# Performance work log

Hardware: AMD Instinct MI355X
Metric: run time of the kernel (lower is better)

Reference implementation:

```python
import jax, jax.numpy as jnp
import numpy as np

N_NODES = 100000
N_EDGES = 1200000
D = 64
N_LAYERS = 3
N_GRAPHS = 128


def setup_inputs() -> dict:
    key = jax.random.key(0)
    ks = jax.random.split(key, 8)
    x = jax.random.normal(ks[0], (N_NODES, D), dtype=jnp.float32)
    edge_index = jax.random.randint(ks[1], (2, N_EDGES), 0, N_NODES, dtype=jnp.int32)
    edge_attr = jax.random.normal(ks[2], (N_EDGES, D), dtype=jnp.float32)
    batch = jnp.sort(jax.random.randint(ks[3], (N_NODES,), 0, N_GRAPHS, dtype=jnp.int32))
    scale = 1.0 / np.sqrt(D)
    W1 = jax.random.normal(ks[4], (N_LAYERS, D, D), dtype=jnp.float32) * scale
    b1 = jnp.zeros((N_LAYERS, D), dtype=jnp.float32)
    W2 = jax.random.normal(ks[5], (N_LAYERS, D, D), dtype=jnp.float32) * scale
    b2 = jnp.zeros((N_LAYERS, D), dtype=jnp.float32)
    Wout = jax.random.normal(ks[6], (D, 1), dtype=jnp.float32) * scale
    bout = jnp.zeros((1,), dtype=jnp.float32)
    return {"x": x, "edge_index": edge_index, "edge_attr": edge_attr, "batch": batch,
            "W1": W1, "b1": b1, "W2": W2, "b2": b2, "Wout": Wout, "bout": bout}


def reference(x, edge_index, edge_attr, batch, W1, b1, W2, b2, Wout, bout):
    n_nodes = x.shape[0]
    src, dst = edge_index[0], edge_index[1]  # j -> i (PyG convention)
    for l in range(N_LAYERS):
        # GINEConv: message = ReLU(x_j + e_ij), sum-aggregate, eps=0
        msg = jax.nn.relu(x[src] + edge_attr)              # [E, D]
        aggr = jax.ops.segment_sum(msg, dst, num_segments=n_nodes)  # [N, D]
        h = x + aggr                                        # (1+eps)*x + aggr, eps=0
        # post-aggregation MLP: Linear -> ReLU -> Linear
        h = jax.nn.relu(h @ W1[l] + b1[l]) @ W2[l] + b2[l]
        x = jax.nn.relu(h)                                  # outer ReLU in GINENet.forward
    pooled = jax.ops.segment_sum(x, batch, num_segments=N_GRAPHS)  # global_add_pool
    out = pooled @ Wout + bout                              # [G, 1]
    return out.squeeze(-1)
```

## Files before the change

### kernel.cpp

```cpp
#include <hip/hip_runtime.h>
#include <hip/hip_bf16.h>

#define D 64

typedef unsigned short u16;
typedef unsigned long long u64;
typedef __attribute__((ext_vector_type(8))) unsigned short u16x8;
typedef __attribute__((ext_vector_type(8))) short bf16x8;
typedef __attribute__((ext_vector_type(4))) float f32x4;

static __device__ __forceinline__ u16 f2bf(float f) {
    unsigned u = __float_as_uint(f);
    unsigned r = (u + 0x7FFFu + ((u >> 16) & 1u)) >> 16;
    return (u16)r;
}
static __device__ __forceinline__ float bf2f(u16 h) {
    return __uint_as_float(((unsigned)h) << 16);
}

__global__ void out_init_kernel(float* __restrict__ out, const float* __restrict__ bout, int G) {
    int i = blockIdx.x * blockDim.x + threadIdx.x;
    if (i < G) out[i] = bout[0];
}

__global__ void deg_hist_kernel(const int* __restrict__ ei, int* __restrict__ deg, int E) {
    int e = blockIdx.x * blockDim.x + threadIdx.x;
    if (e < E) atomicAdd(&deg[ei[E + e]], 1);
}

__global__ __launch_bounds__(1024) void scan1_kernel(
    const int* __restrict__ deg, int* __restrict__ off, int* __restrict__ bsum, int N)
{
    __shared__ int sh[1024];
    int t = threadIdx.x;
    int i = blockIdx.x * 1024 + t;
    int v = (i < N) ? deg[i] : 0;
    sh[t] = v;
    __syncthreads();
#pragma unroll
    for (int o = 1; o < 1024; o <<= 1) {
        int u = (t >= o) ? sh[t - o] : 0;
        __syncthreads();
        sh[t] += u;
        __syncthreads();
    }
    if (i < N) off[i] = sh[t] - v;
    if (t == 1023) bsum[blockIdx.x] = sh[t];
}

__global__ __launch_bounds__(128) void scan2_kernel(
    const int* __restrict__ bsum, int* __restrict__ boff, int nb)
{
    __shared__ int sh[128];
    int t = threadIdx.x;
    int v = (t < nb) ? bsum[t] : 0;
    sh[t] = v;
    __syncthreads();
#pragma unroll
    for (int o = 1; o < 128; o <<= 1) {
        int u = (t >= o) ? sh[t - o] : 0;
        __syncthreads();
        sh[t] += u;
        __syncthreads();
    }
    if (t < nb) boff[t] = sh[t] - v;
}

__global__ void scan3_kernel(int* __restrict__ off, const int* __restrict__ boff, int N) {
    int i = blockIdx.x * blockDim.x + threadIdx.x;
    if (i < N) off[i] += boff[i >> 10];
}

__global__ __launch_bounds__(256) void build_kernel(
    const float* __restrict__ ea, const int* __restrict__ ei,
    const int* __restrict__ off, int* __restrict__ cur,
    int* __restrict__ src_csr, u16* __restrict__ ea_csr, int E)
{
    const int lane = threadIdx.x & 63;
    const int q = lane & 15, g = lane >> 4;
    const long long wv = (long long)blockIdx.x * 4 + (threadIdx.x >> 6);
    const int e = (int)(wv * 4) + g;

    int p = 0, s = 0;
    if (e < E && q == 0) {
        int d = ei[E + e];
        s = ei[e];
        p = off[d] + atomicAdd(&cur[d], 1);
    }
    p = __shfl(p, lane & 48, 64);
    if (e >= E) return;

    float4 v = *(const float4*)&ea[(size_t)e * D + q * 4];
    u64 pk = (u64)f2bf(v.x) | ((u64)f2bf(v.y) << 16)
           | ((u64)f2bf(v.z) << 32) | ((u64)f2bf(v.w) << 48);
    __builtin_nontemporal_store(pk, (u64*)&ea_csr[(size_t)p * D + q * 4]);
    if (q == 0) src_csr[p] = s;
}

__global__ __launch_bounds__(256) void convx_kernel(
    const float* __restrict__ xf, u16* __restrict__ xb, long long n4)
{
    long long i = (long long)blockIdx.x * blockDim.x + threadIdx.x;
    if (i >= n4) return;
    float4 v = ((const float4*)xf)[i];
    ushort4 o;
    o.x = f2bf(v.x); o.y = f2bf(v.y); o.z = f2bf(v.z); o.w = f2bf(v.w);
    ((ushort4*)xb)[i] = o;
}

__global__ __launch_bounds__(256) void aggregate_kernel(
    const u16* __restrict__ xbf, const u16* __restrict__ ea_csr,
    const int* __restrict__ src_csr, const int* __restrict__ off,
    const int* __restrict__ deg, u16* __restrict__ hbf, int N)
{
    const int lane = threadIdx.x & 63;
    const int sub  = lane & 7;
    const int g    = lane >> 3;
    const int n = (blockIdx.x << 2) + (threadIdx.x >> 6);
    if (n >= N) return;

    const int p0 = off[n];
    const int dg = deg[n];

    u16x8 xs;
    if (g == 0) xs = *(const u16x8*)&xbf[(size_t)n * D + sub * 8];

    float a0=0.f,a1=0.f,a2=0.f,a3=0.f,a4=0.f,a5=0.f,a6=0.f,a7=0.f;

    if (dg > 0) {
        const int srcAll = src_csr[p0 + min(lane, dg - 1)];
        const int nct = (dg + 7) >> 3;

        int e0 = min(g, dg - 1);
        int sv = __shfl(srcAll, e0, 64);
        int s0 = sv;
        u16x8 evA = *(const u16x8*)&ea_csr[(size_t)(p0 + e0) * D + sub * 8];
        u16x8 xvA = *(const u16x8*)&xbf[(size_t)s0 * D + sub * 8];
        float mA = (g < dg) ? 1.f : 0.f;

        for (int c = 1; c < nct; ++c) {
            int e1 = min(c * 8 + g, dg - 1);
            int sv1 = __shfl(srcAll, e1 & 63, 64);
            int s1 = (e1 < 64) ? sv1 : src_csr[p0 + e1];
            u16x8 evB = *(const u16x8*)&ea_csr[(size_t)(p0 + e1) * D + sub * 8];
            u16x8 xvB = *(const u16x8*)&xbf[(size_t)s1 * D + sub * 8];
            float mB = (c * 8 + g < dg) ? 1.f : 0.f;

            a0 = fmaf(mA, fmaxf(bf2f(xvA[0]) + bf2f(evA[0]), 0.f), a0);
            a1 = fmaf(mA, fmaxf(bf2f(xvA[1]) + bf2f(evA[1]), 0.f), a1);
            a2 = fmaf(mA, fmaxf(bf2f(xvA[2]) + bf2f(evA[2]), 0.f), a2);
            a3 = fmaf(mA, fmaxf(bf2f(xvA[3]) + bf2f(evA[3]), 0.f), a3);
            a4 = fmaf(mA, fmaxf(bf2f(xvA[4]) + bf2f(evA[4]), 0.f), a4);
            a5 = fmaf(mA, fmaxf(bf2f(xvA[5]) + bf2f(evA[5]), 0.f), a5);
            a6 = fmaf(mA, fmaxf(bf2f(xvA[6]) + bf2f(evA[6]), 0.f), a6);
            a7 = fmaf(mA, fmaxf(bf2f(xvA[7]) + bf2f(evA[7]), 0.f), a7);

            xvA = xvB; evA = evB; mA = mB;
        }
        a0 = fmaf(mA, fmaxf(bf2f(xvA[0]) + bf2f(evA[0]), 0.f), a0);
        a1 = fmaf(mA, fmaxf(bf2f(xvA[1]) + bf2f(evA[1]), 0.f), a1);
        a2 = fmaf(mA, fmaxf(bf2f(xvA[2]) + bf2f(evA[2]), 0.f), a2);
        a3 = fmaf(mA, fmaxf(bf2f(xvA[3]) + bf2f(evA[3]), 0.f), a3);
        a4 = fmaf(mA, fmaxf(bf2f(xvA[4]) + bf2f(evA[4]), 0.f), a4);
        a5 = fmaf(mA, fmaxf(bf2f(xvA[5]) + bf2f(evA[5]), 0.f), a5);
        a6 = fmaf(mA, fmaxf(bf2f(xvA[6]) + bf2f(evA[6]), 0.f), a6);
        a7 = fmaf(mA, fmaxf(bf2f(xvA[7]) + bf2f(evA[7]), 0.f), a7);
    }

#pragma unroll
    for (int o = 8; o < 64; o <<= 1) {
        a0 += __shfl_xor(a0, o, 64);  a1 += __shfl_xor(a1, o, 64);
        a2 += __shfl_xor(a2, o, 64);  a3 += __shfl_xor(a3, o, 64);
        a4 += __shfl_xor(a4, o, 64);  a5 += __shfl_xor(a5, o, 64);
        a6 += __shfl_xor(a6, o, 64);  a7 += __shfl_xor(a7, o, 64);
    }

    if (g == 0) {
        u16x8 ho;
        ho[0] = f2bf(a0 + bf2f(xs[0]));
        ho[1] = f2bf(a1 + bf2f(xs[1]));
        ho[2] = f2bf(a2 + bf2f(xs[2]));
        ho[3] = f2bf(a3 + bf2f(xs[3]));
        ho[4] = f2bf(a4 + bf2f(xs[4]));
        ho[5] = f2bf(a5 + bf2f(xs[5]));
        ho[6] = f2bf(a6 + bf2f(xs[6]));
        ho[7] = f2bf(a7 + bf2f(xs[7]));
        *(u16x8*)&hbf[(size_t)n * D + sub * 8] = ho;
    }
}

template <int LAST>
__global__ __launch_bounds__(256) void mlp_mfma_kernel(
    const u16* __restrict__ hbf, u16* __restrict__ xout,
    const float* __restrict__ W1, const float* __restrict__ b1,
    const float* __restrict__ W2, const float* __restrict__ b2,
    const int* __restrict__ batch, const float* __restrict__ Wout,
    float* __restrict__ out, int N, int ntiles)
{
    __shared__ __align__(16) u16 lds_h[4][16][72];
    __shared__ float pool[128];

    const int lane = threadIdx.x & 63;
    const int wid  = threadIdx.x >> 6;
    const int lr   = lane & 15;
    const int lg   = lane >> 4;

    if (LAST) {
        if (threadIdx.x < 128) pool[threadIdx.x] = 0.f;
        __syncthreads();
    }

    bf16x8 w1f[4][2], w2f[4][2];
#pragma unroll
    for (int nt = 0; nt < 4; ++nt)
#pragma unroll
      for (int ks = 0; ks < 2; ++ks) {
        bf16x8 f1, f2;
#pragma unroll
        for (int j = 0; j < 8; ++j) {
            int k = ks * 32 + lg * 8 + j;
            int c = nt * 16 + lr;
            f1[j] = (short)f2bf(W1[k * D + c]);
            f2[j] = (short)f2bf(W2[k * D + c]);
        }
        w1f[nt][ks] = f1; w2f[nt][ks] = f2;
      }
    float b1v[4], b2v[4], wov[4];
#pragma unroll
    for (int nt = 0; nt < 4; ++nt) {
        b1v[nt] = b1[nt * 16 + lr];
        b2v[nt] = b2[nt * 16 + lr];
        wov[nt] = LAST ? Wout[nt * 16 + lr] : 0.f;
    }

    for (int t = blockIdx.x; t < ntiles; t += gridDim.x) {
        const int m0 = t * 64 + wid * 16;
        if (m0 < N) {
            const int ra = min(m0 + lr, N - 1);
            bf16x8 a0 = *(const bf16x8*)&hbf[(size_t)ra * D + lg * 8];
            bf16x8 a1 = *(const bf16x8*)&hbf[(size_t)ra * D + 32 + lg * 8];

            f32x4 c1[4];
#pragma unroll
            for (int nt = 0; nt < 4; ++nt) {
                f32x4 z = {0.f, 0.f, 0.f, 0.f};
                z = __builtin_amdgcn_mfma_f32_16x16x32_bf16(a0, w1f[nt][0], z, 0, 0, 0);
                z = __builtin_amdgcn_mfma_f32_16x16x32_bf16(a1, w1f[nt][1], z, 0, 0, 0);
                c1[nt] = z;
            }
#pragma unroll
            for (int nt = 0; nt < 4; ++nt)
#pragma unroll
              for (int j = 0; j < 4; ++j) {
                float v = fmaxf(c1[nt][j] + b1v[nt], 0.f);
                lds_h[wid][lg * 4 + j][nt * 16 + lr] = f2bf(v);
              }

            bf16x8 h0 = *(const bf16x8*)&lds_h[wid][lr][lg * 8];
            bf16x8 h1 = *(const bf16x8*)&lds_h[wid][lr][32 + lg * 8];

            f32x4 c2[4];
#pragma unroll
            for (int nt = 0; nt < 4; ++nt) {
                f32x4 z = {0.f, 0.f, 0.f, 0.f};
                z = __builtin_amdgcn_mfma_f32_16x16x32_bf16(h0, w2f[nt][0], z, 0, 0, 0);
                z = __builtin_amdgcn_mfma_f32_16x16x32_bf16(h1, w2f[nt][1], z, 0, 0, 0);
                c2[nt] = z;
            }

            if (!LAST) {
#pragma unroll
                for (int nt = 0; nt < 4; ++nt)
#pragma unroll
                  for (int j = 0; j < 4; ++j) {
                    int gr = m0 + lg * 4 + j;
                    if (gr < N) {
                        float v = fmaxf(c2[nt][j] + b2v[nt], 0.f);
                        xout[(size_t)gr * D + nt * 16 + lr] = f2bf(v);
                    }
                  }
            } else {
                float s0 = 0.f, s1 = 0.f, s2 = 0.f, s3 = 0.f;
#pragma unroll
                for (int nt = 0; nt < 4; ++nt) {
                    s0 = fmaf(fmaxf(c2[nt][0] + b2v[nt], 0.f), wov[nt], s0);
                    s1 = fmaf(fmaxf(c2[nt][1] + b2v[nt], 0.f), wov[nt], s1);
                    s2 = fmaf(fmaxf(c2[nt][2] + b2v[nt], 0.f), wov[nt], s2);
                    s3 = fmaf(fmaxf(c2[nt][3] + b2v[nt], 0.f), wov[nt], s3);
                }
#pragma unroll
                for (int o = 1; o < 16; o <<= 1) {
                    s0 += __shfl_xor(s0, o, 64);
                    s1 += __shfl_xor(s1, o, 64);
                    s2 += __shfl_xor(s2, o, 64);
                    s3 += __shfl_xor(s3, o, 64);
                }
                if (lr == 0) {
                    int gr = m0 + lg * 4;
                    if (gr + 0 < N) atomicAdd(&pool[batch[gr + 0]], s0);
                    if (gr + 1 < N) atomicAdd(&pool[batch[gr + 1]], s1);
                    if (gr + 2 < N) atomicAdd(&pool[batch[gr + 2]], s2);
                    if (gr + 3 < N) atomicAdd(&pool[batch[gr + 3]], s3);
                }
            }
        }
    }

    if (LAST) {
        __syncthreads();
        if (threadIdx.x < 128) {
            float v = pool[threadIdx.x];
            if (v != 0.f) atomicAdd(&out[threadIdx.x], v);
        }
    }
}

extern "C" void kernel_launch(void* const* d_in, const int* in_sizes, int n_in,
                              void* d_out, int out_size, void* d_ws, size_t ws_size,
                              hipStream_t stream) {
    const float* x     = (const float*)d_in[0];
    const int*   ei    = (const int*)d_in[1];
    const float* ea    = (const float*)d_in[2];
    const int*   batch = (const int*)d_in[3];
    const float* W1    = (const float*)d_in[4];
    const float* b1    = (const float*)d_in[5];
    const float* W2    = (const float*)d_in[6];
    const float* b2    = (const float*)d_in[7];
    const float* Wout  = (const float*)d_in[8];
    const float* bout  = (const float*)d_in[9];
    float* out = (float*)d_out;

    const int N = in_sizes[0] / D;
    const int E = in_sizes[1] / 2;
    const int G = out_size;

    char* w = (char*)d_ws;
    u16*   xbfA    = (u16*)w;              w += (size_t)N * D * sizeof(u16);
    u16*   xbfB    = (u16*)w;              w += (size_t)N * D * sizeof(u16);
    u16*   hbf     = (u16*)w;              w += (size_t)N * D * sizeof(u16);
    int*   src_csr = (int*)w;              w += (size_t)E * sizeof(int);
    int*   deg     = (int*)w;              w += (size_t)N * sizeof(int);
    int*   off     = (int*)w;              w += (size_t)N * sizeof(int);
    int*   cur     = (int*)w;              w += (size_t)N * sizeof(int);
    int*   bsum    = (int*)w;              w += 128 * sizeof(int);
    int*   boff    = (int*)w;              w += 128 * sizeof(int);
    u16*   ea_csr  = (u16*)w;

    const int nScanBlocks = (N + 1023) / 1024;
    const int edgeBlocks  = (E + 255) / 256;
    const int buildBlocks = (E + 15) / 16;
    const int aggBlocks   = (N + 3) / 4;

    const long long nx4 = (long long)N * D / 4;
    const int convxBlocks = (int)((nx4 + 255) / 256);

    const int ntiles    = (N + 63) / 64;
    const int mlpBlocks = 782;

    out_init_kernel<<<(G + 127) / 128, 128, 0, stream>>>(out, bout, G);

    hipMemsetAsync(deg, 0, (size_t)N * sizeof(int), stream);
    hipMemsetAsync(cur, 0, (size_t)N * sizeof(int), stream);
    deg_hist_kernel<<<edgeBlocks, 256, 0, stream>>>(ei, deg, E);
    scan1_kernel<<<nScanBlocks, 1024, 0, stream>>>(deg, off, bsum, N);
    scan2_kernel<<<1, 128, 0, stream>>>(bsum, boff, nScanBlocks);
    scan3_kernel<<<(N + 255) / 256, 256, 0, stream>>>(off, boff, N);
    build_kernel<<<buildBlocks, 256, 0, stream>>>(ea, ei, off, cur, src_csr, ea_csr, E);
    convx_kernel<<<convxBlocks, 256, 0, stream>>>(x, xbfA, nx4);

    u16* xcur = xbfA;
    u16* xnxt = xbfB;
    for (int l = 0; l < 3; ++l) {
        aggregate_kernel<<<aggBlocks, 256, 0, stream>>>(xcur, ea_csr, src_csr,
                                                        off, deg, hbf, N);
        if (l < 2) {
            mlp_mfma_kernel<0><<<mlpBlocks, 256, 0, stream>>>(hbf, xnxt,
                W1 + l * D * D, b1 + l * D, W2 + l * D * D, b2 + l * D,
                batch, Wout, out, N, ntiles);
            u16* t = xcur; xcur = xnxt; xnxt = t;
        } else {
            mlp_mfma_kernel<1><<<mlpBlocks, 256, 0, stream>>>(hbf, nullptr,
                W1 + l * D * D, b1 + l * D, W2 + l * D * D, b2 + l * D,
                batch, Wout, out, N, ntiles);
        }
    }
}
```

Measured before the change: 380.7 us.

## Bucket edge-attribute staging by destination range instead of full CSR scatter

Replaces the fully scattered per-edge CSR write of bf16 edge attributes with a two-level bucketing scheme. Edges are counted per 512-node destination bucket per 4096-edge block, per-block bucket bases are computed, and attributes are written to a staging buffer that is ordered by bucket but not fully sorted, with a pos[] indirection stored per CSR slot. The aim is more local, better-coalesced writes in the build phase. In exchange, aggregation needs an extra index load and indirect reads within each bucket, and a serial single-block bases kernel is added.

```diff
diff --git a/kernel.cpp b/kernel.cpp
--- a/kernel.cpp
+++ b/kernel.cpp
@@ -2,6 +2,8 @@
 #include <hip/hip_bf16.h>
 
 #define D 64
+#define BSZ 512
+#define EPB 4096
 
 typedef unsigned short u16;
 typedef unsigned long long u64;
@@ -71,30 +73,72 @@
     if (i < N) off[i] += boff[i >> 10];
 }
 
-__global__ __launch_bounds__(256) void build_kernel(
+__global__ __launch_bounds__(256) void count_kernel(
+    const int* __restrict__ ei, int* __restrict__ counts, int E)
+{
+    __shared__ int cnt[256];
+    for (int i = threadIdx.x; i < 256; i += 256) cnt[i] = 0;
+    __syncthreads();
+    const int e0 = blockIdx.x * EPB;
+    const int e1 = min(e0 + EPB, E);
+    for (int e = e0 + threadIdx.x; e < e1; e += 256)
+        atomicAdd(&cnt[ei[E + e] >> 9], 1);
+    __syncthreads();
+    for (int b = threadIdx.x; b < 256; b += 256)
+        counts[blockIdx.x * 256 + b] = cnt[b];
+}
+
+__global__ __launch_bounds__(256) void bases_kernel(
+    const int* __restrict__ counts, const int* __restrict__ off,
+    int* __restrict__ bases, int nblk, int N)
+{
+    int b = threadIdx.x;
+    int base = ((long long)b * BSZ < N) ? off[b * BSZ] : 0;
+    for (int blk = 0; blk < nblk; ++blk) {
+        bases[blk * 256 + b] = base;
+        base += counts[blk * 256 + b];
+    }
+}
+
+__global__ __launch_bounds__(256) void place_kernel(
     const float* __restrict__ ea, const int* __restrict__ ei,
     const int* __restrict__ off, int* __restrict__ cur,
-    int* __restrict__ src_csr, u16* __restrict__ ea_csr, int E)
-{
+    const int* __restrict__ bases, int* __restrict__ src_csr,
+    int* __restrict__ pos, u16* __restrict__ stage, int E)
+{
+    __shared__ int cur2[256];
+    __shared__ int qs[EPB];
+
+    for (int i = threadIdx.x; i < 256; i += 256)
+        cur2[i] = bases[blockIdx.x * 256 + i];
+    __syncthreads();
+
+    const int e0 = blockIdx.x * EPB;
+    const int e1 = min(e0 + EPB, E);
+
+    for (int e = e0 + threadIdx.x; e < e1; e += 256) {
+        int d = ei[E + e];
+        int s = ei[e];
+        int q = atomicAdd(&cur2[d >> 9], 1);
+        int p = off[d] + atomicAdd(&cur[d], 1);
+        src_csr[p] = s;
+        pos[p]     = q;
+        qs[e - e0] = q;
+    }
+    __syncthreads();
+
     const int lane = threadIdx.x & 63;
-    const int q = lane & 15, g = lane >> 4;
-    const long long wv = (long long)blockIdx.x * 4 + (threadIdx.x >> 6);
-    const int e = (int)(wv * 4) + g;
-
-    int p = 0, s = 0;
-    if (e < E && q == 0) {
-        int d = ei[E + e];
-        s = ei[e];
-        p = off[d] + atomicAdd(&cur[d], 1);
-    }
-    p = __shfl(p, lane & 48, 64);
-    if (e >= E) return;
-
-    float4 v = *(const float4*)&ea[(size_t)e * D + q * 4];
-    u64 pk = (u64)f2bf(v.x) | ((u64)f2bf(v.y) << 16)
-           | ((u64)f2bf(v.z) << 32) | ((u64)f2bf(v.w) << 48);
-    __builtin_nontemporal_store(pk, (u64*)&ea_csr[(size_t)p * D + q * 4]);
-    if (q == 0) src_csr[p] = s;
+    const int qd = lane & 15, g = lane >> 4;
+    const int wid = threadIdx.x >> 6;
+    const int cntE = e1 - e0;
+    for (int i = wid * 4 + g; i < cntE; i += 16) {
+        int e = e0 + i;
+        int q = qs[i];
+        float4 v = *(const float4*)&ea[(size_t)e * D + qd * 4];
+        u64 pk = (u64)f2bf(v.x) | ((u64)f2bf(v.y) << 16)
+               | ((u64)f2bf(v.z) << 32) | ((u64)f2bf(v.w) << 48);
+        *(u64*)&stage[(size_t)q * D + qd * 4] = pk;
+    }
 }
 
 __global__ __launch_bounds__(256) void convx_kernel(
@@ -109,9 +153,10 @@
 }
 
 __global__ __launch_bounds__(256) void aggregate_kernel(
-    const u16* __restrict__ xbf, const u16* __restrict__ ea_csr,
-    const int* __restrict__ src_csr, const int* __restrict__ off,
-    const int* __restrict__ deg, u16* __restrict__ hbf, int N)
+    const u16* __restrict__ xbf, const u16* __restrict__ stage,
+    const int* __restrict__ src_csr, const int* __restrict__ pos,
+    const int* __restrict__ off, const int* __restrict__ deg,
+    u16* __restrict__ hbf, int N)
 {
     const int lane = threadIdx.x & 63;
     const int sub  = lane & 7;
@@ -128,21 +173,25 @@
     float a0=0.f,a1=0.f,a2=0.f,a3=0.f,a4=0.f,a5=0.f,a6=0.f,a7=0.f;
 
     if (dg > 0) {
-        const int srcAll = src_csr[p0 + min(lane, dg - 1)];
+        const int pre    = p0 + min(lane, dg - 1);
+        const int srcAll = src_csr[pre];
+        const int posAll = pos[pre];
         const int nct = (dg + 7) >> 3;
 
         int e0 = min(g, dg - 1);
-        int sv = __shfl(srcAll, e0, 64);
-        int s0 = sv;
-        u16x8 evA = *(const u16x8*)&ea_csr[(size_t)(p0 + e0) * D + sub * 8];
+        int s0 = __shfl(srcAll, e0, 64);
+        int q0 = __shfl(posAll, e0, 64);
+        u16x8 evA = *(const u16x8*)&stage[(size_t)q0 * D + sub * 8];
         u16x8 xvA = *(const u16x8*)&xbf[(size_t)s0 * D + sub * 8];
         float mA = (g < dg) ? 1.f : 0.f;
 
         for (int c = 1; c < nct; ++c) {
             int e1 = min(c * 8 + g, dg - 1);
-            int sv1 = __shfl(srcAll, e1 & 63, 64);
-            int s1 = (e1 < 64) ? sv1 : src_csr[p0 + e1];
-            u16x8 evB = *(const u16x8*)&ea_csr[(size_t)(p0 + e1) * D + sub * 8];
+            int sv = __shfl(srcAll, e1 & 63, 64);
+            int qv = __shfl(posAll, e1 & 63, 64);
+            int s1 = (e1 < 64) ? sv : src_csr[p0 + e1];
+            int q1 = (e1 < 64) ? qv : pos[p0 + e1];
+            u16x8 evB = *(const u16x8*)&stage[(size_t)q1 * D + sub * 8];
             u16x8 xvB = *(const u16x8*)&xbf[(size_t)s1 * D + sub * 8];
             float mB = (c * 8 + g < dg) ? 1.f : 0.f;
 
@@ -333,22 +382,25 @@
     const int N = in_sizes[0] / D;
     const int E = in_sizes[1] / 2;
     const int G = out_size;
+    const int nblk = (E + EPB - 1) / EPB;
 
     char* w = (char*)d_ws;
     u16*   xbfA    = (u16*)w;              w += (size_t)N * D * sizeof(u16);
     u16*   xbfB    = (u16*)w;              w += (size_t)N * D * sizeof(u16);
     u16*   hbf     = (u16*)w;              w += (size_t)N * D * sizeof(u16);
     int*   src_csr = (int*)w;              w += (size_t)E * sizeof(int);
+    int*   pos     = (int*)w;              w += (size_t)E * sizeof(int);
     int*   deg     = (int*)w;              w += (size_t)N * sizeof(int);
     int*   off     = (int*)w;              w += (size_t)N * sizeof(int);
     int*   cur     = (int*)w;              w += (size_t)N * sizeof(int);
+    int*   counts  = (int*)w;              w += (size_t)nblk * 256 * sizeof(int);
+    int*   bases   = (int*)w;              w += (size_t)nblk * 256 * sizeof(int);
     int*   bsum    = (int*)w;              w += 128 * sizeof(int);
     int*   boff    = (int*)w;              w += 128 * sizeof(int);
-    u16*   ea_csr  = (u16*)w;
+    u16*   stage   = (u16*)w;
 
     const int nScanBlocks = (N + 1023) / 1024;
     const int edgeBlocks  = (E + 255) / 256;
-    const int buildBlocks = (E + 15) / 16;
     const int aggBlocks   = (N + 3) / 4;
 
     const long long nx4 = (long long)N * D / 4;
@@ -365,13 +417,16 @@
     scan1_kernel<<<nScanBlocks, 1024, 0, stream>>>(deg, off, bsum, N);
     scan2_kernel<<<1, 128, 0, stream>>>(bsum, boff, nScanBlocks);
     scan3_kernel<<<(N + 255) / 256, 256, 0, stream>>>(off, boff, N);
-    build_kernel<<<buildBlocks, 256, 0, stream>>>(ea, ei, off, cur, src_csr, ea_csr, E);
+    count_kernel<<<nblk, 256, 0, stream>>>(ei, counts, E);
+    bases_kernel<<<1, 256, 0, stream>>>(counts, off, bases, nblk, N);
+    place_kernel<<<nblk, 256, 0, stream>>>(ea, ei, off, cur, bases,
+                                           src_csr, pos, stage, E);
     convx_kernel<<<convxBlocks, 256, 0, stream>>>(x, xbfA, nx4);
 
     u16* xcur = xbfA;
     u16* xnxt = xbfB;
     for (int l = 0; l < 3; ++l) {
-        aggregate_kernel<<<aggBlocks, 256, 0, stream>>>(xcur, ea_csr, src_csr,
+        aggregate_kernel<<<aggBlocks, 256, 0, stream>>>(xcur, stage, src_csr, pos,
                                                         off, deg, hbf, N);
         if (l < 2) {
             mlp_mfma_kernel<0><<<mlpBlocks, 256, 0, stream>>>(hbf, xnxt,
```

Result: slower. 611.6 us (+60.6%).
